# Kernel optimization log

Hardware: AMD Instinct MI355X
Metric: run time of the kernel (lower is better)

Reference implementation:

```python
import jax, jax.numpy as jnp
import numpy as np

CHUNK = 128


def setup_inputs() -> dict:
    key = jax.random.key(0)
    ks = jax.random.split(key, 10)
    B, L, d, n = 4, 2048, 192, 64
    sd = 1.0 / np.sqrt(d)
    return {
        "x": jax.random.normal(ks[0], (B, L, d), dtype=jnp.float32),
        "A_log": -jnp.log(2.0) + 0.1 * jax.random.normal(ks[1], (d,), dtype=jnp.float32),
        "W_B": sd * jax.random.normal(ks[2], (n, d), dtype=jnp.float32),
        "W_C": sd * jax.random.normal(ks[3], (n, d), dtype=jnp.float32),
        "W_dt": sd * jax.random.normal(ks[4], (d, d), dtype=jnp.float32),
        "b_dt": 0.1 * jax.random.normal(ks[5], (d,), dtype=jnp.float32),
        "W_xp": sd * jax.random.normal(ks[6], (2 * d, d), dtype=jnp.float32),
        "b_xp": 0.1 * jax.random.normal(ks[7], (2 * d,), dtype=jnp.float32),
        "W_out": sd * jax.random.normal(ks[8], (d, d), dtype=jnp.float32),
        "b_out": 0.1 * jax.random.normal(ks[9], (d,), dtype=jnp.float32),
    }


def reference(x, A_log, W_B, W_C, W_dt, b_dt, W_xp, b_xp, W_out, b_out):
    p = CHUNK
    b, l, d = x.shape
    n = W_B.shape[0]
    pad = (-l) % p
    xp = jnp.pad(x, ((0, 0), (0, pad), (0, 0))) if pad > 0 else x
    c = xp.shape[1] // p

    A = -jnp.exp(A_log)                                   # (d,)
    proj = xp @ W_xp.T + b_xp                             # (b, Lp, 2d)
    x_bar, z = jnp.split(proj, 2, axis=-1)
    Bm = x_bar @ W_B.T                                    # (b, Lp, n)
    Cm = x_bar @ W_C.T                                    # (b, Lp, n)
    dt = jax.nn.softplus(x_bar @ W_dt.T + b_dt)           # (b, Lp, d)
    A_bar = jnp.exp(dt * A)                               # (b, Lp, d)

    resh = lambda t: t.reshape(b, c, p, t.shape[-1])
    xc, Bc, Cc, Ac = resh(x_bar), resh(Bm), resh(Cm), resh(A_bar)

    # intra-chunk: masked decay matrix M[b,c,i,j,d]
    log_A = jnp.log(jnp.abs(Ac) + 1e-8)
    la_cum = jnp.cumsum(log_A, axis=2)                    # (b,c,p,d)
    log_M = la_cum[:, :, :, None, :] - la_cum[:, :, None, :, :]
    causal = jnp.tril(jnp.ones((p, p), dtype=x.dtype))
    M = jnp.exp(log_M) * causal[None, None, :, :, None]   # (b,c,p,p,d)
    G = jnp.einsum('bcin,bcjn->bcij', Cc, Bc)             # C_i . B_j
    # same math as einsum('bcpn,bcpnd->bcpd', C, einsum('bcijd,bcjnd->bcind', M, B x))
    y_intra = jnp.einsum('bcij,bcijd,bcjd->bcid', G, M, xc)

    # inter-chunk recurrence over chunk states
    chunk_A = jnp.prod(Ac, axis=2)                        # (b,c,d)
    chunk_states = jnp.einsum('bcpn,bcpd->bcnd', Bc, xc * Ac)

    def step(state, inp):
        ca, cs = inp                                       # (b,d), (b,n,d)
        return state * ca[:, None, :] + cs, state          # emit state BEFORE update

    _, prev = jax.lax.scan(
        step,
        jnp.zeros((b, n, d), dtype=x.dtype),
        (jnp.moveaxis(chunk_A, 1, 0), jnp.moveaxis(chunk_states, 1, 0)),
    )
    prev = jnp.moveaxis(prev, 0, 1)                       # (b,c,n,d)
    y_inter = jnp.einsum('bcpn,bcnd->bcpd', Cc, prev)

    y = (y_intra + y_inter).reshape(b, c * p, d)[:, :l]
    y = y * jax.nn.silu(z[:, :l])
    return y @ W_out.T + b_out
```

## Files before the change

kernel.cpp:

```cpp
#include <hip/hip_runtime.h>
#include <math.h>

#define TOK      8192
#define DIM      192
#define NST      64
#define PCHUNK   128
#define NCHUNKS  64
#define CPB      16
#define BATCH    4
#define SUB      32
#define NSUB     4
#define NG       4
#define NPG      16

typedef __attribute__((ext_vector_type(8))) short  bf16x8;
typedef __attribute__((ext_vector_type(4))) float  f32x4;

__device__ __forceinline__ unsigned short f2bf(float f) {
    unsigned int u = __float_as_uint(f);
    u += 0x7fff + ((u >> 16) & 1);
    return (unsigned short)(u >> 16);
}
__device__ __forceinline__ float bf2f(unsigned short h) {
    return __uint_as_float(((unsigned int)h) << 16);
}

#define XU      393216
#define WXPU    18432
#define WOUTU   9216
#define CAST_U  (XU + WXPU + WOUTU)
#define WCOMB_N 61440
#define PREP_N  (CAST_U + WCOMB_N + 320)

__global__ __launch_bounds__(256)
void prep_kernel(const float* __restrict__ x,   const float* __restrict__ Wxp,
                 const float* __restrict__ WB,  const float* __restrict__ WC,
                 const float* __restrict__ Wdt, const float* __restrict__ Wout,
                 const float* __restrict__ b_xp, const float* __restrict__ b_dt,
                 unsigned short* __restrict__ xb,     unsigned short* __restrict__ wxpb,
                 unsigned short* __restrict__ woutb,  unsigned short* __restrict__ wcombb,
                 float* __restrict__ biasC)
{
    int u = blockIdx.x * 256 + threadIdx.x;
    if (u < CAST_U) {
        const float* src; unsigned short* dst; int idx;
        if      (u < XU)          { src = x;    dst = xb;    idx = u; }
        else if (u < XU + WXPU)   { src = Wxp;  dst = wxpb;  idx = u - XU; }
        else                      { src = Wout; dst = woutb; idx = u - XU - WXPU; }
        float4 v = *(const float4*)(src + (size_t)idx * 4);
        ushort4 r; r.x = f2bf(v.x); r.y = f2bf(v.y); r.z = f2bf(v.z); r.w = f2bf(v.w);
        *(ushort4*)(dst + (size_t)idx * 4) = r;
    } else if (u < CAST_U + WCOMB_N) {
        int idx = u - CAST_U;
        int n = idx / DIM, k = idx % DIM;
        const float* wr = (n < 64) ? WB + (size_t)n * DIM
                        : (n < 128) ? WC + (size_t)(n - 64) * DIM
                                    : Wdt + (size_t)(n - 128) * DIM;
        float acc = 0.f;
        for (int j = 0; j < DIM; ++j)
            acc = fmaf(wr[j], Wxp[(size_t)j * DIM + k], acc);
        wcombb[(size_t)n * DIM + k] = f2bf(acc);
    } else if (u < PREP_N) {
        int n = u - CAST_U - WCOMB_N;
        const float* wr = (n < 64) ? WB + (size_t)n * DIM
                        : (n < 128) ? WC + (size_t)(n - 64) * DIM
                                    : Wdt + (size_t)(n - 128) * DIM;
        float acc = 0.f;
        for (int j = 0; j < DIM; ++j)
            acc = fmaf(wr[j], b_xp[j], acc);
        if (n >= 128) acc += b_dt[n - 128];
        biasC[n] = acc;
    }
}

__device__ __forceinline__
void mfma_64x64(const unsigned short* __restrict__ X, int ldx,
                const unsigned short* __restrict__ W, int K,
                int m_wave, int n0, int lr, int kg, f32x4 acc[4][4])
{
    for (int k0 = 0; k0 < K; k0 += 32) {
        bf16x8 af[4], bfr[4];
        #pragma unroll
        for (int mi = 0; mi < 4; ++mi)
            af[mi] = *(const bf16x8*)(X + (size_t)(m_wave + mi*16 + lr) * ldx + k0 + kg*8);
        #pragma unroll
        for (int ni = 0; ni < 4; ++ni)
            bfr[ni] = *(const bf16x8*)(W + (size_t)(n0 + ni*16 + lr) * K + k0 + kg*8);
        #pragma unroll
        for (int mi = 0; mi < 4; ++mi)
            #pragma unroll
            for (int ni = 0; ni < 4; ++ni)
                acc[mi][ni] = __builtin_amdgcn_mfma_f32_16x16x32_bf16(
                                  af[mi], bfr[ni], acc[mi][ni], 0, 0, 0);
    }
}

__global__ __launch_bounds__(256)
void xz_gemm(const unsigned short* __restrict__ xb,
             const unsigned short* __restrict__ wxpb,
             const float* __restrict__ b_xp,
             float* __restrict__ xbar, float* __restrict__ zarr)
{
    const int lane = threadIdx.x & 63, wave = threadIdx.x >> 6;
    const int m_wave = blockIdx.x * 256 + wave * 64;
    const int n0 = blockIdx.y * 64;
    const int lr = lane & 15, kg = lane >> 4;
    f32x4 acc[4][4] = {};
    mfma_64x64(xb, DIM, wxpb, DIM, m_wave, n0, lr, kg, acc);
    float* dst = (n0 < DIM) ? xbar : zarr;
    int cofs = (n0 < DIM) ? 0 : DIM;
    #pragma unroll
    for (int ni = 0; ni < 4; ++ni) {
        int col = n0 + ni*16 + lr;
        float bias = b_xp[col];
        #pragma unroll
        for (int mi = 0; mi < 4; ++mi)
            #pragma unroll
            for (int r = 0; r < 4; ++r) {
                int row = m_wave + mi*16 + kg*4 + r;
                dst[(size_t)row * DIM + col - cofs] = acc[mi][ni][r] + bias;
            }
    }
}

__global__ __launch_bounds__(256)
void bcdt_gemm(const unsigned short* __restrict__ xb,
               const unsigned short* __restrict__ wcombb,
               const float* __restrict__ biasC, const float* __restrict__ A_log,
               float* __restrict__ BC, float* __restrict__ Abar)
{
    const int lane = threadIdx.x & 63, wave = threadIdx.x >> 6;
    const int m_wave = blockIdx.x * 256 + wave * 64;
    const int n0 = blockIdx.y * 64;
    const int lr = lane & 15, kg = lane >> 4;
    f32x4 acc[4][4] = {};
    mfma_64x64(xb, DIM, wcombb, DIM, m_wave, n0, lr, kg, acc);
    if (n0 < 128) {
        #pragma unroll
        for (int ni = 0; ni < 4; ++ni) {
            int col = n0 + ni*16 + lr;
            float bias = biasC[col];
            #pragma unroll
            for (int mi = 0; mi < 4; ++mi)
                #pragma unroll
                for (int r = 0; r < 4; ++r) {
                    int row = m_wave + mi*16 + kg*4 + r;
                    BC[(size_t)row * 128 + col] = acc[mi][ni][r] + bias;
                }
        }
    } else {
        #pragma unroll
        for (int ni = 0; ni < 4; ++ni) {
            int col = n0 + ni*16 + lr;
            int c2 = col - 128;
            float bias = biasC[col];
            float Av = -expf(A_log[c2]);
            #pragma unroll
            for (int mi = 0; mi < 4; ++mi)
                #pragma unroll
                for (int r = 0; r < 4; ++r) {
                    int row = m_wave + mi*16 + kg*4 + r;
                    float v = acc[mi][ni][r] + bias;
                    float sp = (v > 20.f) ? v : log1pf(expf(v));
                    Abar[(size_t)row * DIM + c2] = expf(sp * Av);
                }
        }
    }
}

__global__ __launch_bounds__(256)
void out_gemm(const unsigned short* __restrict__ ygb,
              const unsigned short* __restrict__ woutb,
              const float* __restrict__ b_out, float* __restrict__ out)
{
    const int lane = threadIdx.x & 63, wave = threadIdx.x >> 6;
    const int m_wave = blockIdx.x * 256 + wave * 64;
    const int n0 = blockIdx.y * 64;
    const int lr = lane & 15, kg = lane >> 4;
    f32x4 acc[4][4] = {};
    mfma_64x64(ygb, DIM, woutb, DIM, m_wave, n0, lr, kg, acc);
    #pragma unroll
    for (int ni = 0; ni < 4; ++ni) {
        int col = n0 + ni*16 + lr;
        float bias = b_out[col];
        #pragma unroll
        for (int mi = 0; mi < 4; ++mi)
            #pragma unroll
            for (int r = 0; r < 4; ++r) {
                int row = m_wave + mi*16 + kg*4 + r;
                out[(size_t)row * DIM + col] = acc[mi][ni][r] + bias;
            }
    }
}

__global__ __launch_bounds__(192)
void state_kernel(const float* __restrict__ xbar,
                  const float* __restrict__ Abar,
                  const float* __restrict__ Bm,
                  unsigned short* __restrict__ S,
                  unsigned short* __restrict__ R,
                  float* __restrict__ dprod)
{
    int bc = blockIdx.x, s = blockIdx.y, g = blockIdx.z;
    int dd = threadIdx.x;
    int t0 = bc * PCHUNK + s * SUB;
    __shared__ float Bs[SUB][NPG];
    if (threadIdx.x < SUB * NPG / 4) {
        int row = threadIdx.x >> 2, c4 = threadIdx.x & 3;
        *(float4*)&Bs[row][c4 * 4] =
            *(const float4*)(Bm + (size_t)(t0 + row) * 128 + g * NPG + c4 * 4);
    }
    __syncthreads();
    float H[NPG] = {}, Rr[NPG] = {};
    float cp = 1.f;
    float a_cur = Abar[(size_t)t0 * DIM + dd] + 1e-8f;
    float x_cur = xbar[(size_t)t0 * DIM + dd];
    for (int i = 0; i < SUB; ++i) {
        float a_nxt = 0.f, x_nxt = 0.f;
        if (i + 1 < SUB) {
            a_nxt = Abar[(size_t)(t0 + i + 1) * DIM + dd] + 1e-8f;
            x_nxt = xbar[(size_t)(t0 + i + 1) * DIM + dd];
        }
        cp *= a_cur;
        float4 b0 = *(const float4*)&Bs[i][0];
        float4 b1 = *(const float4*)&Bs[i][4];
        float4 b2 = *(const float4*)&Bs[i][8];
        float4 b3 = *(const float4*)&Bs[i][12];
        float bb[NPG] = {b0.x,b0.y,b0.z,b0.w, b1.x,b1.y,b1.z,b1.w,
                         b2.x,b2.y,b2.z,b2.w, b3.x,b3.y,b3.z,b3.w};
        #pragma unroll
        for (int j = 0; j < NPG; ++j) {
            float u = bb[j] * x_cur;
            H[j]  = fmaf(a_cur, H[j], u);
            Rr[j] = fmaf(u, a_cur, Rr[j]);
        }
        a_cur = a_nxt; x_cur = x_nxt;
    }
    size_t base = (((size_t)(bc * NSUB + s)) * NST + g * NPG) * DIM + dd;
    #pragma unroll
    for (int j = 0; j < NPG; ++j) {
        S[base + (size_t)j * DIM] = f2bf(H[j]);
        R[base + (size_t)j * DIM] = f2bf(Rr[j]);
    }
    if (g == 0) dprod[(size_t)(bc * PCHUNK / SUB + s) * DIM + dd] = cp;
}

__global__ __launch_bounds__(256)
void reduce_kernel(const float* __restrict__ dprod,
                   const unsigned short* __restrict__ R,
                   float* __restrict__ cA,
                   float* __restrict__ Rsum)
{
    int u = blockIdx.x * 256 + threadIdx.x;
    const int NR = NCHUNKS * NST * 48;
    if (u < NR) {
        int dd = (u % 48) * 4;
        int nn = (u / 48) % NST;
        int bc = u / (48 * NST);
        const size_t Q2 = (size_t)NST * DIM;
        size_t so = ((size_t)(bc * NSUB) * NST + nn) * DIM + dd;
        float4 acc = {0.f, 0.f, 0.f, 0.f};
        #pragma unroll
        for (int s = 0; s < NSUB; ++s) {
            ushort4 v = *(const ushort4*)(R + so + (size_t)s * Q2);
            acc.x += bf2f(v.x); acc.y += bf2f(v.y);
            acc.z += bf2f(v.z); acc.w += bf2f(v.w);
        }
        *(float4*)(Rsum + ((size_t)bc * NST + nn) * DIM + dd) = acc;
    } else if (u < NR + NCHUNKS * 48) {
        int v = u - NR;
        int dd = (v % 48) * 4;
        int bc = v / 48;
        float4 acc = {1.f, 1.f, 1.f, 1.f};
        #pragma unroll
        for (int s = 0; s < NSUB; ++s) {
            float4 dp = *(const float4*)(dprod + (size_t)(bc * NSUB + s) * DIM + dd);
            acc.x *= dp.x; acc.y *= dp.y; acc.z *= dp.z; acc.w *= dp.w;
        }
        *(float4*)(cA + (size_t)bc * DIM + dd) = acc;
    }
}

__global__ __launch_bounds__(256)
void scan_kernel(const float* __restrict__ cA,
                 const float* __restrict__ Rsum,
                 float* __restrict__ prev)
{
    int v = blockIdx.x * 256 + threadIdx.x;
    if (v >= BATCH * NST * 48) return;
    int dd = (v % 48) * 4;
    int nn = (v / 48) % NST;
    int b  = v / (48 * NST);
    int bc0 = b * CPB;
    float4 st = {0.f, 0.f, 0.f, 0.f};
    float4 a_cur = *(const float4*)(cA + (size_t)bc0 * DIM + dd);
    float4 r_cur = *(const float4*)(Rsum + ((size_t)bc0 * NST + nn) * DIM + dd);
    for (int c = 0; c < CPB; ++c) {
        int bc = bc0 + c;
        float4 a_nxt = {0,0,0,0}, r_nxt = {0,0,0,0};
        if (c + 1 < CPB) {
            a_nxt = *(const float4*)(cA + (size_t)(bc + 1) * DIM + dd);
            r_nxt = *(const float4*)(Rsum + ((size_t)(bc + 1) * NST + nn) * DIM + dd);
        }
        *(float4*)(prev + ((size_t)bc * NST + nn) * DIM + dd) = st;
        st.x = fmaf(st.x, a_cur.x, r_cur.x);
        st.y = fmaf(st.y, a_cur.y, r_cur.y);
        st.z = fmaf(st.z, a_cur.z, r_cur.z);
        st.w = fmaf(st.w, a_cur.w, r_cur.w);
        a_cur = a_nxt; r_cur = r_nxt;
    }
}

__global__ __launch_bounds__(192)
void intra_kernel(const float* __restrict__ xbar,
                  const float* __restrict__ Abar,
                  const float* __restrict__ BC,
                  const float* __restrict__ prev,
                  const unsigned short* __restrict__ S,
                  const float* __restrict__ dprod,
                  unsigned short* __restrict__ p_y)
{
    int bc = blockIdx.x, s = blockIdx.y, g = blockIdx.z;
    int dd = threadIdx.x;
    int t0 = bc * PCHUNK + s * SUB;
    __shared__ float Bs[SUB][NPG];
    __shared__ float Cs[SUB][NPG];
    {
        int nunits = SUB * NPG / 4;
        for (int idx = threadIdx.x; idx < 2 * nunits; idx += 192) {
            int m = idx >= nunits;
            int q = idx - m * nunits;
            int row = q >> 2, c4 = q & 3;
            const float* src = BC + (size_t)(t0 + row) * 128
                             + (m ? 64 : 0) + g * NPG + c4 * 4;
            float4 v = *(const float4*)src;
            if (m) *(float4*)&Cs[row][c4 * 4] = v;
            else   *(float4*)&Bs[row][c4 * 4] = v;
        }
    }
    float H[NPG] = {}, P[NPG];
    for (int k = 0; k < s; ++k) {
        float dpk = dprod[(size_t)(bc * NSUB + k) * DIM + dd];
        size_t sb = (((size_t)(bc * NSUB + k)) * NST + g * NPG) * DIM + dd;
        #pragma unroll
        for (int j = 0; j < NPG; ++j)
            H[j] = fmaf(H[j], dpk, bf2f(S[sb + (size_t)j * DIM]));
    }
    #pragma unroll
    for (int j = 0; j < NPG; ++j)
        P[j] = prev[((size_t)bc * NST + g * NPG + j) * DIM + dd];
    __syncthreads();

    float a_cur = Abar[(size_t)t0 * DIM + dd] + 1e-8f;
    float x_cur = xbar[(size_t)t0 * DIM + dd];
    for (int i = 0; i < SUB; ++i) {
        int t = t0 + i;
        float a_nxt = 0.f, x_nxt = 0.f;
        if (i + 1 < SUB) {
            a_nxt = Abar[(size_t)(t + 1) * DIM + dd] + 1e-8f;
            x_nxt = xbar[(size_t)(t + 1) * DIM + dd];
        }
        float4 b0 = *(const float4*)&Bs[i][0];
        float4 b1 = *(const float4*)&Bs[i][4];
        float4 b2 = *(const float4*)&Bs[i][8];
        float4 b3 = *(const float4*)&Bs[i][12];
        float4 c0 = *(const float4*)&Cs[i][0];
        float4 c1 = *(const float4*)&Cs[i][4];
        float4 c2 = *(const float4*)&Cs[i][8];
        float4 c3 = *(const float4*)&Cs[i][12];
        float bb[NPG] = {b0.x,b0.y,b0.z,b0.w, b1.x,b1.y,b1.z,b1.w,
                         b2.x,b2.y,b2.z,b2.w, b3.x,b3.y,b3.z,b3.w};
        float cc[NPG] = {c0.x,c0.y,c0.z,c0.w, c1.x,c1.y,c1.z,c1.w,
                         c2.x,c2.y,c2.z,c2.w, c3.x,c3.y,c3.z,c3.w};
        float ya[4] = {0.f, 0.f, 0.f, 0.f};
        #pragma unroll
        for (int j = 0; j < NPG; ++j) {
            H[j] = fmaf(a_cur, H[j], bb[j] * x_cur);
            ya[j & 3] = fmaf(cc[j], H[j] + P[j], ya[j & 3]);
        }
        p_y[((size_t)g * TOK + t) * DIM + dd] = f2bf((ya[0] + ya[1]) + (ya[2] + ya[3]));
        a_cur = a_nxt; x_cur = x_nxt;
    }
}

__global__ __launch_bounds__(256)
void gate_kernel(const unsigned short* __restrict__ p_y,
                 const float* __restrict__ zarr,
                 unsigned short* __restrict__ ygb)
{
    int v = blockIdx.x * 256 + threadIdx.x;
    if (v >= TOK * 48) return;
    int t = v / 48;
    int dd = (v % 48) * 4;
    const size_t Q = (size_t)TOK * DIM;
    size_t off = (size_t)t * DIM + dd;
    float acc[4] = {0.f, 0.f, 0.f, 0.f};
    #pragma unroll
    for (int gidx = 0; gidx < NG; ++gidx) {
        ushort4 y = *(const ushort4*)(p_y + off + (size_t)gidx * Q);
        acc[0] += bf2f(y.x); acc[1] += bf2f(y.y);
        acc[2] += bf2f(y.z); acc[3] += bf2f(y.w);
    }
    float4 z = *(const float4*)(zarr + off);
    ushort4 r;
    r.x = f2bf(acc[0] * (z.x / (1.f + expf(-z.x))));
    r.y = f2bf(acc[1] * (z.y / (1.f + expf(-z.y))));
    r.z = f2bf(acc[2] * (z.z / (1.f + expf(-z.z))));
    r.w = f2bf(acc[3] * (z.w / (1.f + expf(-z.w))));
    *(ushort4*)(ygb + off) = r;
}

extern "C" void kernel_launch(void* const* d_in, const int* in_sizes, int n_in,
                              void* d_out, int out_size, void* d_ws, size_t ws_size,
                              hipStream_t stream)
{
    (void)in_sizes; (void)n_in; (void)out_size; (void)ws_size;
    const float* x     = (const float*)d_in[0];
    const float* A_log = (const float*)d_in[1];
    const float* W_B   = (const float*)d_in[2];
    const float* W_C   = (const float*)d_in[3];
    const float* W_dt  = (const float*)d_in[4];
    const float* b_dt  = (const float*)d_in[5];
    const float* W_xp  = (const float*)d_in[6];
    const float* b_xp  = (const float*)d_in[7];
    const float* W_out = (const float*)d_in[8];
    const float* b_out = (const float*)d_in[9];
    float* out = (float*)d_out;

    char* w = (char*)d_ws;
    auto take = [&](size_t bytes) { char* p = w; w += (bytes + 255) & ~(size_t)255; return p; };
    unsigned short* xb     = (unsigned short*)take((size_t)TOK*DIM*2);
    unsigned short* wxpb   = (unsigned short*)take((size_t)384*DIM*2);
    unsigned short* woutb  = (unsigned short*)take((size_t)DIM*DIM*2);
    unsigned short* wcombb = (unsigned short*)take((size_t)320*DIM*2);
    float*          biasC  = (float*)         take((size_t)320*4);
    float*          xbar   = (float*)         take((size_t)TOK*DIM*4);
    float*          zarr   = (float*)         take((size_t)TOK*DIM*4);
    float*          BC     = (float*)         take((size_t)TOK*128*4);
    float*          Abar   = (float*)         take((size_t)TOK*DIM*4);
    float*          dprod  = (float*)         take((size_t)NCHUNKS*NSUB*DIM*4);
    float*          cAc    = (float*)         take((size_t)NCHUNKS*DIM*4);
    float*          prev   = (float*)         take((size_t)NCHUNKS*NST*DIM*4);
    float*          Rsum   = (float*)         take((size_t)NCHUNKS*NST*DIM*4);
    unsigned short* Sarr   = (unsigned short*)take((size_t)NCHUNKS*NSUB*NST*DIM*2);
    unsigned short* Rarr   = (unsigned short*)take((size_t)NCHUNKS*NSUB*NST*DIM*2);
    unsigned short* p_y    = (unsigned short*)take((size_t)NG*TOK*DIM*2);
    unsigned short* ygb    = (unsigned short*)take((size_t)TOK*DIM*2);

    dim3 blk(256);

    prep_kernel<<<dim3((PREP_N + 255)/256), blk, 0, stream>>>(
        x, W_xp, W_B, W_C, W_dt, W_out, b_xp, b_dt, xb, wxpb, woutb, wcombb, biasC);
    xz_gemm<<<dim3(TOK/256, 384/64), blk, 0, stream>>>(xb, wxpb, b_xp, xbar, zarr);
    bcdt_gemm<<<dim3(TOK/256, 320/64), blk, 0, stream>>>(xb, wcombb, biasC, A_log, BC, Abar);
    state_kernel<<<dim3(NCHUNKS, NSUB, NG), dim3(192), 0, stream>>>(
        xbar, Abar, BC, Sarr, Rarr, dprod);
    reduce_kernel<<<dim3((NCHUNKS*NST*48 + NCHUNKS*48 + 255)/256), blk, 0, stream>>>(
        dprod, Rarr, cAc, Rsum);
    scan_kernel<<<dim3((BATCH*NST*48 + 255)/256), blk, 0, stream>>>(cAc, Rsum, prev);
    intra_kernel<<<dim3(NCHUNKS, NSUB, NG), dim3(192), 0, stream>>>(
        xbar, Abar, BC, prev, Sarr, dprod, p_y);
    gate_kernel<<<dim3((TOK*48 + 255)/256), blk, 0, stream>>>(p_y, zarr, ygb);
    out_gemm<<<dim3(TOK/256, DIM/64), blk, 0, stream>>>(ygb, woutb, b_out, out);
}
```

Baseline: 184.9 us.

## Merge projection GEMMs, fold reduce into scan, keep states in fp32, vectorize weight fold

Concatenates W_xp and the folded B/C/dt weights into one 704-row matrix so a single GEMM launch produces xbar, z, B, C and Abar. The separate reduce kernel is removed and the scan now sums the four sub-chunk states and multiplies the decay products itself, with one-step prefetch. Sub-chunk states S and R are stored as fp32 instead of bf16, which removes conversions and rounding but doubles their memory traffic. The prep kernel's weight-fold loop now computes four outputs per thread with float4 loads.

```diff
diff --git a/kernel.cpp b/kernel.cpp
--- a/kernel.cpp
+++ b/kernel.cpp
@@ -29,47 +29,60 @@
 #define WXPU    18432
 #define WOUTU   9216
 #define CAST_U  (XU + WXPU + WOUTU)
-#define WCOMB_N 61440
-#define PREP_N  (CAST_U + WCOMB_N + 320)
+#define FOLD_U  15360
+#define PREP_N  (CAST_U + FOLD_U + 704)
 
 __global__ __launch_bounds__(256)
 void prep_kernel(const float* __restrict__ x,   const float* __restrict__ Wxp,
                  const float* __restrict__ WB,  const float* __restrict__ WC,
                  const float* __restrict__ Wdt, const float* __restrict__ Wout,
                  const float* __restrict__ b_xp, const float* __restrict__ b_dt,
-                 unsigned short* __restrict__ xb,     unsigned short* __restrict__ wxpb,
-                 unsigned short* __restrict__ woutb,  unsigned short* __restrict__ wcombb,
-                 float* __restrict__ biasC)
+                 unsigned short* __restrict__ xb,
+                 unsigned short* __restrict__ bigW,
+                 unsigned short* __restrict__ woutb,
+                 float* __restrict__ biasAll)
 {
     int u = blockIdx.x * 256 + threadIdx.x;
     if (u < CAST_U) {
         const float* src; unsigned short* dst; int idx;
-        if      (u < XU)          { src = x;    dst = xb;    idx = u; }
-        else if (u < XU + WXPU)   { src = Wxp;  dst = wxpb;  idx = u - XU; }
-        else                      { src = Wout; dst = woutb; idx = u - XU - WXPU; }
+        if      (u < XU)        { src = x;    dst = xb;    idx = u; }
+        else if (u < XU + WXPU) { src = Wxp;  dst = bigW;  idx = u - XU; }
+        else                    { src = Wout; dst = woutb; idx = u - XU - WXPU; }
         float4 v = *(const float4*)(src + (size_t)idx * 4);
         ushort4 r; r.x = f2bf(v.x); r.y = f2bf(v.y); r.z = f2bf(v.z); r.w = f2bf(v.w);
         *(ushort4*)(dst + (size_t)idx * 4) = r;
-    } else if (u < CAST_U + WCOMB_N) {
+    } else if (u < CAST_U + FOLD_U) {
         int idx = u - CAST_U;
-        int n = idx / DIM, k = idx % DIM;
+        int n = idx / 48, k4 = idx % 48;
         const float* wr = (n < 64) ? WB + (size_t)n * DIM
                         : (n < 128) ? WC + (size_t)(n - 64) * DIM
                                     : Wdt + (size_t)(n - 128) * DIM;
-        float acc = 0.f;
-        for (int j = 0; j < DIM; ++j)
-            acc = fmaf(wr[j], Wxp[(size_t)j * DIM + k], acc);
-        wcombb[(size_t)n * DIM + k] = f2bf(acc);
+        float4 acc = {0.f, 0.f, 0.f, 0.f};
+        for (int j = 0; j < DIM; ++j) {
+            float w = wr[j];
+            float4 xp = *(const float4*)(Wxp + (size_t)j * DIM + k4 * 4);
+            acc.x = fmaf(w, xp.x, acc.x); acc.y = fmaf(w, xp.y, acc.y);
+            acc.z = fmaf(w, xp.z, acc.z); acc.w = fmaf(w, xp.w, acc.w);
+        }
+        ushort4 r; r.x = f2bf(acc.x); r.y = f2bf(acc.y); r.z = f2bf(acc.z); r.w = f2bf(acc.w);
+        *(ushort4*)(bigW + (size_t)(384 + n) * DIM + k4 * 4) = r;
     } else if (u < PREP_N) {
-        int n = u - CAST_U - WCOMB_N;
+        int col = u - CAST_U - FOLD_U;
+        if (col < 384) { biasAll[col] = b_xp[col]; return; }
+        int n = col - 384;
         const float* wr = (n < 64) ? WB + (size_t)n * DIM
                         : (n < 128) ? WC + (size_t)(n - 64) * DIM
                                     : Wdt + (size_t)(n - 128) * DIM;
-        float acc = 0.f;
-        for (int j = 0; j < DIM; ++j)
-            acc = fmaf(wr[j], b_xp[j], acc);
+        float a0 = 0.f, a1 = 0.f, a2 = 0.f, a3 = 0.f;
+        for (int j = 0; j < DIM; j += 4) {
+            a0 = fmaf(wr[j+0], b_xp[j+0], a0);
+            a1 = fmaf(wr[j+1], b_xp[j+1], a1);
+            a2 = fmaf(wr[j+2], b_xp[j+2], a2);
+            a3 = fmaf(wr[j+3], b_xp[j+3], a3);
+        }
+        float acc = (a0 + a1) + (a2 + a3);
         if (n >= 128) acc += b_dt[n - 128];
-        biasC[n] = acc;
+        biasAll[col] = acc;
     }
 }
 
@@ -96,64 +109,52 @@
 }
 
 __global__ __launch_bounds__(256)
-void xz_gemm(const unsigned short* __restrict__ xb,
-             const unsigned short* __restrict__ wxpb,
-             const float* __restrict__ b_xp,
-             float* __restrict__ xbar, float* __restrict__ zarr)
+void gemm_all(const unsigned short* __restrict__ xb,
+              const unsigned short* __restrict__ bigW,
+              const float* __restrict__ biasAll, const float* __restrict__ A_log,
+              float* __restrict__ xbar, float* __restrict__ zarr,
+              float* __restrict__ BC, float* __restrict__ Abar)
 {
     const int lane = threadIdx.x & 63, wave = threadIdx.x >> 6;
     const int m_wave = blockIdx.x * 256 + wave * 64;
     const int n0 = blockIdx.y * 64;
     const int lr = lane & 15, kg = lane >> 4;
     f32x4 acc[4][4] = {};
-    mfma_64x64(xb, DIM, wxpb, DIM, m_wave, n0, lr, kg, acc);
-    float* dst = (n0 < DIM) ? xbar : zarr;
-    int cofs = (n0 < DIM) ? 0 : DIM;
-    #pragma unroll
-    for (int ni = 0; ni < 4; ++ni) {
-        int col = n0 + ni*16 + lr;
-        float bias = b_xp[col];
-        #pragma unroll
-        for (int mi = 0; mi < 4; ++mi)
-            #pragma unroll
-            for (int r = 0; r < 4; ++r) {
-                int row = m_wave + mi*16 + kg*4 + r;
-                dst[(size_t)row * DIM + col - cofs] = acc[mi][ni][r] + bias;
-            }
-    }
-}
-
-__global__ __launch_bounds__(256)
-void bcdt_gemm(const unsigned short* __restrict__ xb,
-               const unsigned short* __restrict__ wcombb,
-               const float* __restrict__ biasC, const float* __restrict__ A_log,
-               float* __restrict__ BC, float* __restrict__ Abar)
-{
-    const int lane = threadIdx.x & 63, wave = threadIdx.x >> 6;
-    const int m_wave = blockIdx.x * 256 + wave * 64;
-    const int n0 = blockIdx.y * 64;
-    const int lr = lane & 15, kg = lane >> 4;
-    f32x4 acc[4][4] = {};
-    mfma_64x64(xb, DIM, wcombb, DIM, m_wave, n0, lr, kg, acc);
-    if (n0 < 128) {
+    mfma_64x64(xb, DIM, bigW, DIM, m_wave, n0, lr, kg, acc);
+    if (n0 < 384) {
+        float* dst = (n0 < 192) ? xbar : zarr;
+        int cofs = (n0 < 192) ? 0 : 192;
         #pragma unroll
         for (int ni = 0; ni < 4; ++ni) {
             int col = n0 + ni*16 + lr;
-            float bias = biasC[col];
+            float bias = biasAll[col];
             #pragma unroll
             for (int mi = 0; mi < 4; ++mi)
                 #pragma unroll
                 for (int r = 0; r < 4; ++r) {
                     int row = m_wave + mi*16 + kg*4 + r;
-                    BC[(size_t)row * 128 + col] = acc[mi][ni][r] + bias;
+                    dst[(size_t)row * DIM + col - cofs] = acc[mi][ni][r] + bias;
                 }
         }
-    } else {
+    } else if (n0 < 512) {
         #pragma unroll
         for (int ni = 0; ni < 4; ++ni) {
             int col = n0 + ni*16 + lr;
-            int c2 = col - 128;
-            float bias = biasC[col];
+            float bias = biasAll[col];
+            #pragma unroll
+            for (int mi = 0; mi < 4; ++mi)
+                #pragma unroll
+                for (int r = 0; r < 4; ++r) {
+                    int row = m_wave + mi*16 + kg*4 + r;
+                    BC[(size_t)row * 128 + col - 384] = acc[mi][ni][r] + bias;
+                }
+        }
+    } else {
+        #pragma unroll
+        for (int ni = 0; ni < 4; ++ni) {
+            int col = n0 + ni*16 + lr;
+            int c2 = col - 512;
+            float bias = biasAll[col];
             float Av = -expf(A_log[c2]);
             #pragma unroll
             for (int mi = 0; mi < 4; ++mi)
@@ -197,8 +198,8 @@
 void state_kernel(const float* __restrict__ xbar,
                   const float* __restrict__ Abar,
                   const float* __restrict__ Bm,
-                  unsigned short* __restrict__ S,
-                  unsigned short* __restrict__ R,
+                  float* __restrict__ S,
+                  float* __restrict__ R,
                   float* __restrict__ dprod)
 {
     int bc = blockIdx.x, s = blockIdx.y, g = blockIdx.z;
@@ -239,51 +240,15 @@
     size_t base = (((size_t)(bc * NSUB + s)) * NST + g * NPG) * DIM + dd;
     #pragma unroll
     for (int j = 0; j < NPG; ++j) {
-        S[base + (size_t)j * DIM] = f2bf(H[j]);
-        R[base + (size_t)j * DIM] = f2bf(Rr[j]);
-    }
-    if (g == 0) dprod[(size_t)(bc * PCHUNK / SUB + s) * DIM + dd] = cp;
+        S[base + (size_t)j * DIM] = H[j];
+        R[base + (size_t)j * DIM] = Rr[j];
+    }
+    if (g == 0) dprod[(size_t)(bc * NSUB + s) * DIM + dd] = cp;
 }
 
 __global__ __launch_bounds__(256)
-void reduce_kernel(const float* __restrict__ dprod,
-                   const unsigned short* __restrict__ R,
-                   float* __restrict__ cA,
-                   float* __restrict__ Rsum)
-{
-    int u = blockIdx.x * 256 + threadIdx.x;
-    const int NR = NCHUNKS * NST * 48;
-    if (u < NR) {
-        int dd = (u % 48) * 4;
-        int nn = (u / 48) % NST;
-        int bc = u / (48 * NST);
-        const size_t Q2 = (size_t)NST * DIM;
-        size_t so = ((size_t)(bc * NSUB) * NST + nn) * DIM + dd;
-        float4 acc = {0.f, 0.f, 0.f, 0.f};
-        #pragma unroll
-        for (int s = 0; s < NSUB; ++s) {
-            ushort4 v = *(const ushort4*)(R + so + (size_t)s * Q2);
-            acc.x += bf2f(v.x); acc.y += bf2f(v.y);
-            acc.z += bf2f(v.z); acc.w += bf2f(v.w);
-        }
-        *(float4*)(Rsum + ((size_t)bc * NST + nn) * DIM + dd) = acc;
-    } else if (u < NR + NCHUNKS * 48) {
-        int v = u - NR;
-        int dd = (v % 48) * 4;
-        int bc = v / 48;
-        float4 acc = {1.f, 1.f, 1.f, 1.f};
-        #pragma unroll
-        for (int s = 0; s < NSUB; ++s) {
-            float4 dp = *(const float4*)(dprod + (size_t)(bc * NSUB + s) * DIM + dd);
-            acc.x *= dp.x; acc.y *= dp.y; acc.z *= dp.z; acc.w *= dp.w;
-        }
-        *(float4*)(cA + (size_t)bc * DIM + dd) = acc;
-    }
-}
-
-__global__ __launch_bounds__(256)
-void scan_kernel(const float* __restrict__ cA,
-                 const float* __restrict__ Rsum,
+void scan_kernel(const float* __restrict__ dprod,
+                 const float* __restrict__ R,
                  float* __restrict__ prev)
 {
     int v = blockIdx.x * 256 + threadIdx.x;
@@ -292,22 +257,46 @@
     int nn = (v / 48) % NST;
     int b  = v / (48 * NST);
     int bc0 = b * CPB;
+    const size_t Q2 = (size_t)NST * DIM;
+    float4 rv[NSUB], dv[NSUB];
+    {
+        size_t so = ((size_t)(bc0 * NSUB) * NST + nn) * DIM + dd;
+        size_t po = (size_t)(bc0 * NSUB) * DIM + dd;
+        #pragma unroll
+        for (int s = 0; s < NSUB; ++s) {
+            rv[s] = *(const float4*)(R + so + (size_t)s * Q2);
+            dv[s] = *(const float4*)(dprod + po + (size_t)s * DIM);
+        }
+    }
     float4 st = {0.f, 0.f, 0.f, 0.f};
-    float4 a_cur = *(const float4*)(cA + (size_t)bc0 * DIM + dd);
-    float4 r_cur = *(const float4*)(Rsum + ((size_t)bc0 * NST + nn) * DIM + dd);
     for (int c = 0; c < CPB; ++c) {
         int bc = bc0 + c;
-        float4 a_nxt = {0,0,0,0}, r_nxt = {0,0,0,0};
+        float4 rn[NSUB], dn[NSUB];
         if (c + 1 < CPB) {
-            a_nxt = *(const float4*)(cA + (size_t)(bc + 1) * DIM + dd);
-            r_nxt = *(const float4*)(Rsum + ((size_t)(bc + 1) * NST + nn) * DIM + dd);
-        }
+            size_t so = ((size_t)((bc + 1) * NSUB) * NST + nn) * DIM + dd;
+            size_t po = (size_t)((bc + 1) * NSUB) * DIM + dd;
+            #pragma unroll
+            for (int s = 0; s < NSUB; ++s) {
+                rn[s] = *(const float4*)(R + so + (size_t)s * Q2);
+                dn[s] = *(const float4*)(dprod + po + (size_t)s * DIM);
+            }
+        }
+        float4 Rs, cA;
+        Rs.x = (rv[0].x + rv[1].x) + (rv[2].x + rv[3].x);
+        Rs.y = (rv[0].y + rv[1].y) + (rv[2].y + rv[3].y);
+        Rs.z = (rv[0].z + rv[1].z) + (rv[2].z + rv[3].z);
+        Rs.w = (rv[0].w + rv[1].w) + (rv[2].w + rv[3].w);
+        cA.x = (dv[0].x * dv[1].x) * (dv[2].x * dv[3].x);
+        cA.y = (dv[0].y * dv[1].y) * (dv[2].y * dv[3].y);
+        cA.z = (dv[0].z * dv[1].z) * (dv[2].z * dv[3].z);
+        cA.w = (dv[0].w * dv[1].w) * (dv[2].w * dv[3].w);
         *(float4*)(prev + ((size_t)bc * NST + nn) * DIM + dd) = st;
-        st.x = fmaf(st.x, a_cur.x, r_cur.x);
-        st.y = fmaf(st.y, a_cur.y, r_cur.y);
-        st.z = fmaf(st.z, a_cur.z, r_cur.z);
-        st.w = fmaf(st.w, a_cur.w, r_cur.w);
-        a_cur = a_nxt; r_cur = r_nxt;
+        st.x = fmaf(st.x, cA.x, Rs.x);
+        st.y = fmaf(st.y, cA.y, Rs.y);
+        st.z = fmaf(st.z, cA.z, Rs.z);
+        st.w = fmaf(st.w, cA.w, Rs.w);
+        #pragma unroll
+        for (int s = 0; s < NSUB; ++s) { rv[s] = rn[s]; dv[s] = dn[s]; }
     }
 }
 
@@ -316,7 +305,7 @@
                   const float* __restrict__ Abar,
                   const float* __restrict__ BC,
                   const float* __restrict__ prev,
-                  const unsigned short* __restrict__ S,
+                  const float* __restrict__ S,
                   const float* __restrict__ dprod,
                   unsigned short* __restrict__ p_y)
 {
@@ -344,7 +333,7 @@
         size_t sb = (((size_t)(bc * NSUB + k)) * NST + g * NPG) * DIM + dd;
         #pragma unroll
         for (int j = 0; j < NPG; ++j)
-            H[j] = fmaf(H[j], dpk, bf2f(S[sb + (size_t)j * DIM]));
+            H[j] = fmaf(H[j], dpk, S[sb + (size_t)j * DIM]);
     }
     #pragma unroll
     for (int j = 0; j < NPG; ++j)
@@ -430,34 +419,29 @@
     char* w = (char*)d_ws;
     auto take = [&](size_t bytes) { char* p = w; w += (bytes + 255) & ~(size_t)255; return p; };
     unsigned short* xb     = (unsigned short*)take((size_t)TOK*DIM*2);
-    unsigned short* wxpb   = (unsigned short*)take((size_t)384*DIM*2);
+    unsigned short* bigW   = (unsigned short*)take((size_t)704*DIM*2);
     unsigned short* woutb  = (unsigned short*)take((size_t)DIM*DIM*2);
-    unsigned short* wcombb = (unsigned short*)take((size_t)320*DIM*2);
-    float*          biasC  = (float*)         take((size_t)320*4);
+    float*          biasAll= (float*)         take((size_t)704*4);
     float*          xbar   = (float*)         take((size_t)TOK*DIM*4);
     float*          zarr   = (float*)         take((size_t)TOK*DIM*4);
     float*          BC     = (float*)         take((size_t)TOK*128*4);
     float*          Abar   = (float*)         take((size_t)TOK*DIM*4);
     float*          dprod  = (float*)         take((size_t)NCHUNKS*NSUB*DIM*4);
-    float*          cAc    = (float*)         take((size_t)NCHUNKS*DIM*4);
     float*          prev   = (float*)         take((size_t)NCHUNKS*NST*DIM*4);
-    float*          Rsum   = (float*)         take((size_t)NCHUNKS*NST*DIM*4);
-    unsigned short* Sarr   = (unsigned short*)take((size_t)NCHUNKS*NSUB*NST*DIM*2);
-    unsigned short* Rarr   = (unsigned short*)take((size_t)NCHUNKS*NSUB*NST*DIM*2);
+    float*          Sarr   = (float*)         take((size_t)NCHUNKS*NSUB*NST*DIM*4);
+    float*          Rarr   = (float*)         take((size_t)NCHUNKS*NSUB*NST*DIM*4);
     unsigned short* p_y    = (unsigned short*)take((size_t)NG*TOK*DIM*2);
     unsigned short* ygb    = (unsigned short*)take((size_t)TOK*DIM*2);
 
     dim3 blk(256);
 
     prep_kernel<<<dim3((PREP_N + 255)/256), blk, 0, stream>>>(
-        x, W_xp, W_B, W_C, W_dt, W_out, b_xp, b_dt, xb, wxpb, woutb, wcombb, biasC);
-    xz_gemm<<<dim3(TOK/256, 384/64), blk, 0, stream>>>(xb, wxpb, b_xp, xbar, zarr);
-    bcdt_gemm<<<dim3(TOK/256, 320/64), blk, 0, stream>>>(xb, wcombb, biasC, A_log, BC, Abar);
+        x, W_xp, W_B, W_C, W_dt, W_out, b_xp, b_dt, xb, bigW, woutb, biasAll);
+    gemm_all<<<dim3(TOK/256, 704/64), blk, 0, stream>>>(
+        xb, bigW, biasAll, A_log, xbar, zarr, BC, Abar);
     state_kernel<<<dim3(NCHUNKS, NSUB, NG), dim3(192), 0, stream>>>(
         xbar, Abar, BC, Sarr, Rarr, dprod);
-    reduce_kernel<<<dim3((NCHUNKS*NST*48 + NCHUNKS*48 + 255)/256), blk, 0, stream>>>(
-        dprod, Rarr, cAc, Rsum);
-    scan_kernel<<<dim3((BATCH*NST*48 + 255)/256), blk, 0, stream>>>(cAc, Rsum, prev);
+    scan_kernel<<<dim3((BATCH*NST*48 + 255)/256), blk, 0, stream>>>(dprod, Rarr, prev);
     intra_kernel<<<dim3(NCHUNKS, NSUB, NG), dim3(192), 0, stream>>>(
         xbar, Abar, BC, prev, Sarr, dprod, p_y);
     gate_kernel<<<dim3((TOK*48 + 255)/256), blk, 0, stream>>>(p_y, zarr, ygb);
```

After: 186.0 us. About the same (+0.6%).
